# Performance work log

Hardware: AMD Instinct MI355X
Metric: run time of the kernel (lower is better)

The kernel has to match this reference:

```python
import jax, jax.numpy as jnp
import numpy as np


def setup_inputs() -> dict:
    key = jax.random.key(0)
    ks = jax.random.split(key, 7)
    B, T, I, H, O = 128, 1024, 256, 512, 128
    s_i = 1.0 / np.sqrt(I)
    s_h = 1.0 / np.sqrt(H)
    return {
        "x": jax.random.normal(ks[0], (B, T, I), dtype=jnp.float32),
        "W_ih": jax.random.normal(ks[1], (3 * H, I), dtype=jnp.float32) * s_i,
        "W_hh": jax.random.normal(ks[2], (3 * H, H), dtype=jnp.float32) * s_h,
        "b_ih": jax.random.normal(ks[3], (3 * H,), dtype=jnp.float32) * s_h,
        "b_hh": jax.random.normal(ks[4], (3 * H,), dtype=jnp.float32) * s_h,
        "fc_W": jax.random.normal(ks[5], (O, H), dtype=jnp.float32) * s_h,
        "fc_b": jax.random.normal(ks[6], (O,), dtype=jnp.float32) * s_h,
    }


def reference(x, W_ih, W_hh, b_ih, b_hh, fc_W, fc_b):
    # x: [B, T, I]. Standard torch GRUCell recurrence, scanned over time.
    B = x.shape[0]
    H = W_hh.shape[1]
    h0 = jnp.zeros((B, H), dtype=x.dtype)

    def step(h, xt):
        gx = xt @ W_ih.T + b_ih            # [B, 3H]
        gh = h @ W_hh.T + b_hh             # [B, 3H]
        gx_r, gx_z, gx_n = jnp.split(gx, 3, axis=-1)
        gh_r, gh_z, gh_n = jnp.split(gh, 3, axis=-1)
        r = jax.nn.sigmoid(gx_r + gh_r)
        z = jax.nn.sigmoid(gx_z + gh_z)
        n = jnp.tanh(gx_n + r * gh_n)
        h_new = (1.0 - z) * n + z * h
        return h_new, None

    xs = jnp.swapaxes(x, 0, 1)             # [T, B, I]
    h_last, _ = jax.lax.scan(step, h0, xs)
    return h_last @ fc_W.T + fc_b          # [B, O]
```

## Files before the change

### kernel.cpp

```cpp
#include <hip/hip_runtime.h>

#define B_ 128
#define T_ 1024
#define I_ 256
#define H_ 512
#define O_ 128

#define BGROUPS 4
#define ROWS 32
#define CGROUPS 32
#define HC 16
#define NBLK (BGROUPS*CGROUPS)
#define NTHR 512

#define HSLAB (B_*(H_/2))
#define FLAGS_OFF (2*HSLAB)
#define WS_INIT_BYTES ((2*HSLAB + T_*BGROUPS*CGROUPS)*4)

#define LDS_BYTES 32768

typedef __attribute__((ext_vector_type(8))) short short8;
typedef __attribute__((ext_vector_type(4))) float f32x4;

__device__ __forceinline__ unsigned int bf16rne(float f) {
    unsigned int u = __builtin_bit_cast(unsigned int, f);
    u += 0x7fffu + ((u >> 16) & 1u);
    return u >> 16;
}
__device__ __forceinline__ short8 pack8(float4 a, float4 b) {
    short8 r;
    r[0]=(short)bf16rne(a.x); r[1]=(short)bf16rne(a.y); r[2]=(short)bf16rne(a.z); r[3]=(short)bf16rne(a.w);
    r[4]=(short)bf16rne(b.x); r[5]=(short)bf16rne(b.y); r[6]=(short)bf16rne(b.z); r[7]=(short)bf16rne(b.w);
    return r;
}
__device__ __forceinline__ short8 cvt8(const float* p) {
    return pack8(*(const float4*)p, *(const float4*)(p + 4));
}

__global__ __launch_bounds__(NTHR, 1)
void gru_mfma(const float* __restrict__ x,
              const float* __restrict__ Wih,
              const float* __restrict__ Whh,
              const float* __restrict__ bih,
              const float* __restrict__ bhh,
              unsigned int* __restrict__ hslab,
              unsigned int* __restrict__ flags)
{
    __shared__ __align__(16) char smem[LDS_BYTES];

    const int tid  = threadIdx.x;
    const int lane = tid & 63;
    const int g    = blockIdx.x >> 5;
    const int cg   = blockIdx.x & 31;
    const int rb0  = g * ROWS;
    const int hc0  = cg * HC;

    const int wv = tid >> 6;
    const int mt = wv & 1;
    const int kq = wv >> 1;

    short8 BX[2][3], BH[4][3];
#pragma unroll
    for (int xk = 0; xk < 2; ++xk) {
        int kb = (kq * 2 + xk) * 32 + ((lane >> 4) << 3);
#pragma unroll
        for (int nt = 0; nt < 3; ++nt)
            BX[xk][nt] = cvt8(Wih + (nt * H_ + hc0 + (lane & 15)) * I_ + kb);
    }
#pragma unroll
    for (int hk = 0; hk < 4; ++hk) {
        int kb = (kq * 4 + hk) * 32 + ((lane >> 4) << 3);
#pragma unroll
        for (int nt = 0; nt < 3; ++nt)
            BH[hk][nt] = cvt8(Whh + (nt * H_ + hc0 + (lane & 15)) * H_ + kb);
    }

    const int arow = rb0 + mt * 16 + (lane & 15);
    const int kch  = lane >> 4;

    const int frow = tid >> 4;
    const int fcl  = tid & 15;
    const int j    = hc0 + fcl;
    const float bR  = bih[j] + bhh[j];
    const float bZ  = bih[H_ + j] + bhh[H_ + j];
    const float bNx = bih[2 * H_ + j];
    const float bNh = bhh[2 * H_ + j];
    const int mtf  = frow >> 4;
    const int r16  = frow & 15;
    const int fbase = ((((r16 >> 2) << 4) | fcl) << 2) + (r16 & 3);
    float hprev = 0.f;

    const float* xp0 = x + (arow * T_) * I_ + (kq * 2) * 32 + kch * 8;
    const float* xp1 = xp0 + 32;
    float4 pxa0 = *(const float4*)xp0, pxa1 = *(const float4*)(xp0 + 4);
    float4 pxb0 = *(const float4*)xp1, pxb1 = *(const float4*)(xp1 + 4);
    xp0 += I_; xp1 += I_;

#pragma unroll 1
    for (int t = 0; t < T_; ++t) {
        if (t > 0) {
            const unsigned int* fl = flags + ((t - 1) * BGROUPS + g) * CGROUPS;
            if (tid < 64) {
                unsigned int v;
                do {
                    v = __hip_atomic_load(fl + (lane & 31), __ATOMIC_RELAXED, __HIP_MEMORY_SCOPE_AGENT);
                } while (!__all((int)(v != 0)));
            }
        }
        __syncthreads();

        const unsigned int* hrowp = hslab + (t & 1) * HSLAB + arow * (H_ / 2) + kch * 4;
        unsigned long long hq[8];
#pragma unroll
        for (int hk = 0; hk < 4; ++hk) {
            const unsigned long long* p =
                (const unsigned long long*)(hrowp + (kq * 4 + hk) * 16);
            hq[2 * hk]     = __hip_atomic_load(p,     __ATOMIC_RELAXED, __HIP_MEMORY_SCOPE_AGENT);
            hq[2 * hk + 1] = __hip_atomic_load(p + 1, __ATOMIC_RELAXED, __HIP_MEMORY_SCOPE_AGENT);
        }

        f32x4 accR = {0.f, 0.f, 0.f, 0.f}, accZ = accR, accNX = accR, accNH = accR;
        {
            short8 ax0 = pack8(pxa0, pxa1);
            short8 ax1 = pack8(pxb0, pxb1);
            accR  = __builtin_amdgcn_mfma_f32_16x16x32_bf16(ax0, BX[0][0], accR, 0, 0, 0);
            accZ  = __builtin_amdgcn_mfma_f32_16x16x32_bf16(ax0, BX[0][1], accZ, 0, 0, 0);
            accNX = __builtin_amdgcn_mfma_f32_16x16x32_bf16(ax0, BX[0][2], accNX, 0, 0, 0);
            accR  = __builtin_amdgcn_mfma_f32_16x16x32_bf16(ax1, BX[1][0], accR, 0, 0, 0);
            accZ  = __builtin_amdgcn_mfma_f32_16x16x32_bf16(ax1, BX[1][1], accZ, 0, 0, 0);
            accNX = __builtin_amdgcn_mfma_f32_16x16x32_bf16(ax1, BX[1][2], accNX, 0, 0, 0);
        }
#pragma unroll
        for (int hk = 0; hk < 4; ++hk) {
            union { unsigned long long q[2]; short8 s; } u;
            u.q[0] = hq[2 * hk]; u.q[1] = hq[2 * hk + 1];
            accR  = __builtin_amdgcn_mfma_f32_16x16x32_bf16(u.s, BH[hk][0], accR, 0, 0, 0);
            accZ  = __builtin_amdgcn_mfma_f32_16x16x32_bf16(u.s, BH[hk][1], accZ, 0, 0, 0);
            accNH = __builtin_amdgcn_mfma_f32_16x16x32_bf16(u.s, BH[hk][2], accNH, 0, 0, 0);
        }

        {
            char* cb = smem + wv * 1024 + lane * 16;
            *(f32x4*)(cb +     0) = accR;
            *(f32x4*)(cb +  8192) = accZ;
            *(f32x4*)(cb + 16384) = accNX;
            *(f32x4*)(cb + 24576) = accNH;
        }
        __syncthreads();

        {
            const float* CB = (const float*)smem;
            float sr = bR, sz = bZ, sxn = bNx, shn = bNh;
#pragma unroll
            for (int q = 0; q < 4; ++q) {
                int base = (q * 2 + mtf) * 256 + fbase;
                sr  += CB[base];
                sz  += CB[2048 + base];
                sxn += CB[4096 + base];
                shn += CB[6144 + base];
            }
            float r = 1.f / (1.f + __expf(-sr));
            float z = 1.f / (1.f + __expf(-sz));
            float e2 = __expf(2.f * (sxn + r * shn));
            float n = 1.f - 2.f / (e2 + 1.f);
            float hnew = (1.f - z) * n + z * hprev;
            hprev = hnew;
            unsigned int hb = bf16rne(hnew);
            unsigned int ob = (unsigned int)__shfl_xor((int)hb, 1);
            if (!(fcl & 1)) {
                unsigned int pk = (hb & 0xffffu) | (ob << 16);
                __hip_atomic_store(hslab + ((t + 1) & 1) * HSLAB + (rb0 + frow) * (H_ / 2) + (j >> 1),
                                   pk, __ATOMIC_RELAXED, __HIP_MEMORY_SCOPE_AGENT);
            }
        }
        __syncthreads();

        if (tid == 0)
            __hip_atomic_store(flags + (t * BGROUPS + g) * CGROUPS + cg, 1u,
                               __ATOMIC_RELAXED, __HIP_MEMORY_SCOPE_AGENT);
        if (t + 1 < T_) {
            pxa0 = *(const float4*)xp0; pxa1 = *(const float4*)(xp0 + 4);
            pxb0 = *(const float4*)xp1; pxb1 = *(const float4*)(xp1 + 4);
            xp0 += I_; xp1 += I_;
        }
    }
}

__global__ __launch_bounds__(256)
void fc_kernel(const unsigned int* __restrict__ hp,
               const float* __restrict__ fcW,
               const float* __restrict__ fcb,
               float* __restrict__ out)
{
    int gid = blockIdx.x * 256 + threadIdx.x;
    int b = gid >> 7, o = gid & 127;
    const unsigned int* hr = hp + b * (H_ / 2);
    const float* wr = fcW + o * H_;
    float acc = 0.f;
#pragma unroll 8
    for (int i = 0; i < H_ / 2; i += 4) {
        uint4 v = *(const uint4*)(hr + i);
        float4 w0 = *(const float4*)(wr + 2 * i);
        float4 w1 = *(const float4*)(wr + 2 * i + 4);
        acc += __builtin_bit_cast(float, v.x << 16)          * w0.x
             + __builtin_bit_cast(float, v.x & 0xffff0000u)  * w0.y
             + __builtin_bit_cast(float, v.y << 16)          * w0.z
             + __builtin_bit_cast(float, v.y & 0xffff0000u)  * w0.w
             + __builtin_bit_cast(float, v.z << 16)          * w1.x
             + __builtin_bit_cast(float, v.z & 0xffff0000u)  * w1.y
             + __builtin_bit_cast(float, v.w << 16)          * w1.z
             + __builtin_bit_cast(float, v.w & 0xffff0000u)  * w1.w;
    }
    out[gid] = acc + fcb[o];
}

extern "C" void kernel_launch(void* const* d_in, const int* in_sizes, int n_in,
                              void* d_out, int out_size, void* d_ws, size_t ws_size,
                              hipStream_t stream)
{
    const float* x   = (const float*)d_in[0];
    const float* Wih = (const float*)d_in[1];
    const float* Whh = (const float*)d_in[2];
    const float* bih = (const float*)d_in[3];
    const float* bhh = (const float*)d_in[4];
    const float* fcW = (const float*)d_in[5];
    const float* fcb = (const float*)d_in[6];
    float* out = (float*)d_out;

    unsigned int* hslab = (unsigned int*)d_ws;
    unsigned int* flags = hslab + FLAGS_OFF;

    hipMemsetAsync(d_ws, 0, WS_INIT_BYTES, stream);

    hipLaunchKernelGGL(gru_mfma, dim3(NBLK), dim3(NTHR), 0, stream,
                       x, Wih, Whh, bih, bhh, hslab, flags);

    hipLaunchKernelGGL(fc_kernel, dim3((B_ * O_) / 256), dim3(256), 0, stream,
                       hslab, fcW, fcb, out);
}
```

Baseline: 4.016 ms.

## Replace per-step flag barrier with step-tagged 64-bit hidden-state words

Each packed bf16 pair of the hidden state is now stored in a 64-bit word whose upper half holds the timestep, so consumers spin directly on the data they need instead of polling a separate flag array and then reading the hidden state. This removes the producer-side barrier plus flag store and the consumer flag-poll round trip from each recurrent step, and each wave only waits on its own slice. In exchange, hidden-state traffic doubles and each lane issues more atomic loads. The FC kernel is adapted to skip the tag halves.

Result: slower. 7.746 ms (+92.9%).

```diff
diff --git a/kernel.cpp b/kernel.cpp
--- a/kernel.cpp
+++ b/kernel.cpp
@@ -13,9 +13,8 @@
 #define NBLK (BGROUPS*CGROUPS)
 #define NTHR 512
 
-#define HSLAB (B_*(H_/2))
-#define FLAGS_OFF (2*HSLAB)
-#define WS_INIT_BYTES ((2*HSLAB + T_*BGROUPS*CGROUPS)*4)
+#define HSLAB64 (B_*(H_/2))
+#define WS_INIT_BYTES (2*HSLAB64*8)
 
 #define LDS_BYTES 32768
 
@@ -35,6 +34,9 @@
 }
 __device__ __forceinline__ short8 cvt8(const float* p) {
     return pack8(*(const float4*)p, *(const float4*)(p + 4));
+}
+__device__ __forceinline__ unsigned long long ald64(const unsigned long long* p) {
+    return __hip_atomic_load(p, __ATOMIC_RELAXED, __HIP_MEMORY_SCOPE_AGENT);
 }
 
 __global__ __launch_bounds__(NTHR, 1)
@@ -43,8 +45,7 @@
               const float* __restrict__ Whh,
               const float* __restrict__ bih,
               const float* __restrict__ bhh,
-              unsigned int* __restrict__ hslab,
-              unsigned int* __restrict__ flags)
+              unsigned long long* __restrict__ hslab)
 {
     __shared__ __align__(16) char smem[LDS_BYTES];
 
@@ -96,27 +97,31 @@
     float4 pxb0 = *(const float4*)xp1, pxb1 = *(const float4*)(xp1 + 4);
     xp0 += I_; xp1 += I_;
 
+    const int hfo = arow * (H_ / 2) + kch * 4;
+
 #pragma unroll 1
     for (int t = 0; t < T_; ++t) {
-        if (t > 0) {
-            const unsigned int* fl = flags + ((t - 1) * BGROUPS + g) * CGROUPS;
-            if (tid < 64) {
-                unsigned int v;
-                do {
-                    v = __hip_atomic_load(fl + (lane & 31), __ATOMIC_RELAXED, __HIP_MEMORY_SCOPE_AGENT);
-                } while (!__all((int)(v != 0)));
-            }
-        }
-        __syncthreads();
-
-        const unsigned int* hrowp = hslab + (t & 1) * HSLAB + arow * (H_ / 2) + kch * 4;
-        unsigned long long hq[8];
+        const unsigned long long* hb64 = hslab + (t & 1) * HSLAB64 + hfo;
+        const unsigned int want = (unsigned int)t;
+        unsigned long long v[16];
 #pragma unroll
         for (int hk = 0; hk < 4; ++hk) {
-            const unsigned long long* p =
-                (const unsigned long long*)(hrowp + (kq * 4 + hk) * 16);
-            hq[2 * hk]     = __hip_atomic_load(p,     __ATOMIC_RELAXED, __HIP_MEMORY_SCOPE_AGENT);
-            hq[2 * hk + 1] = __hip_atomic_load(p + 1, __ATOMIC_RELAXED, __HIP_MEMORY_SCOPE_AGENT);
+            const unsigned long long* p = hb64 + (kq * 4 + hk) * 16;
+            v[4*hk+0] = ald64(p + 0);
+            v[4*hk+1] = ald64(p + 1);
+            v[4*hk+2] = ald64(p + 2);
+            v[4*hk+3] = ald64(p + 3);
+        }
+        for (;;) {
+            bool ok = true;
+#pragma unroll
+            for (int i = 0; i < 16; ++i)
+                if ((unsigned int)(v[i] >> 32) != want) ok = false;
+            if (ok) break;
+#pragma unroll
+            for (int i = 0; i < 16; ++i)
+                if ((unsigned int)(v[i] >> 32) != want)
+                    v[i] = ald64(hb64 + ((i >> 2) + kq * 4) * 16 + (i & 3));
         }
 
         f32x4 accR = {0.f, 0.f, 0.f, 0.f}, accZ = accR, accNX = accR, accNH = accR;
@@ -132,13 +137,17 @@
         }
 #pragma unroll
         for (int hk = 0; hk < 4; ++hk) {
-            union { unsigned long long q[2]; short8 s; } u;
-            u.q[0] = hq[2 * hk]; u.q[1] = hq[2 * hk + 1];
+            union { unsigned int w[4]; short8 s; } u;
+            u.w[0] = (unsigned int)v[4*hk+0];
+            u.w[1] = (unsigned int)v[4*hk+1];
+            u.w[2] = (unsigned int)v[4*hk+2];
+            u.w[3] = (unsigned int)v[4*hk+3];
             accR  = __builtin_amdgcn_mfma_f32_16x16x32_bf16(u.s, BH[hk][0], accR, 0, 0, 0);
             accZ  = __builtin_amdgcn_mfma_f32_16x16x32_bf16(u.s, BH[hk][1], accZ, 0, 0, 0);
             accNH = __builtin_amdgcn_mfma_f32_16x16x32_bf16(u.s, BH[hk][2], accNH, 0, 0, 0);
         }
 
+        __syncthreads();
         {
             char* cb = smem + wv * 1024 + lane * 16;
             *(f32x4*)(cb +     0) = accR;
@@ -168,16 +177,13 @@
             unsigned int hb = bf16rne(hnew);
             unsigned int ob = (unsigned int)__shfl_xor((int)hb, 1);
             if (!(fcl & 1)) {
-                unsigned int pk = (hb & 0xffffu) | (ob << 16);
-                __hip_atomic_store(hslab + ((t + 1) & 1) * HSLAB + (rb0 + frow) * (H_ / 2) + (j >> 1),
+                unsigned long long pk = (unsigned long long)((hb & 0xffffu) | ((ob & 0xffffu) << 16))
+                                      | ((unsigned long long)(unsigned int)(t + 1) << 32);
+                __hip_atomic_store(hslab + ((t + 1) & 1) * HSLAB64 + (rb0 + frow) * (H_ / 2) + (j >> 1),
                                    pk, __ATOMIC_RELAXED, __HIP_MEMORY_SCOPE_AGENT);
             }
         }
-        __syncthreads();
-
-        if (tid == 0)
-            __hip_atomic_store(flags + (t * BGROUPS + g) * CGROUPS + cg, 1u,
-                               __ATOMIC_RELAXED, __HIP_MEMORY_SCOPE_AGENT);
+
         if (t + 1 < T_) {
             pxa0 = *(const float4*)xp0; pxa1 = *(const float4*)(xp0 + 4);
             pxb0 = *(const float4*)xp1; pxb1 = *(const float4*)(xp1 + 4);
@@ -187,29 +193,24 @@
 }
 
 __global__ __launch_bounds__(256)
-void fc_kernel(const unsigned int* __restrict__ hp,
+void fc_kernel(const unsigned long long* __restrict__ hp,
                const float* __restrict__ fcW,
                const float* __restrict__ fcb,
                float* __restrict__ out)
 {
     int gid = blockIdx.x * 256 + threadIdx.x;
     int b = gid >> 7, o = gid & 127;
-    const unsigned int* hr = hp + b * (H_ / 2);
+    const unsigned long long* hr = hp + b * (H_ / 2);
     const float* wr = fcW + o * H_;
     float acc = 0.f;
 #pragma unroll 8
-    for (int i = 0; i < H_ / 2; i += 4) {
+    for (int i = 0; i < H_ / 2; i += 2) {
         uint4 v = *(const uint4*)(hr + i);
-        float4 w0 = *(const float4*)(wr + 2 * i);
-        float4 w1 = *(const float4*)(wr + 2 * i + 4);
-        acc += __builtin_bit_cast(float, v.x << 16)          * w0.x
-             + __builtin_bit_cast(float, v.x & 0xffff0000u)  * w0.y
-             + __builtin_bit_cast(float, v.y << 16)          * w0.z
-             + __builtin_bit_cast(float, v.y & 0xffff0000u)  * w0.w
-             + __builtin_bit_cast(float, v.z << 16)          * w1.x
-             + __builtin_bit_cast(float, v.z & 0xffff0000u)  * w1.y
-             + __builtin_bit_cast(float, v.w << 16)          * w1.z
-             + __builtin_bit_cast(float, v.w & 0xffff0000u)  * w1.w;
+        float4 w = *(const float4*)(wr + 2 * i);
+        acc += __builtin_bit_cast(float, v.x << 16)          * w.x
+             + __builtin_bit_cast(float, v.x & 0xffff0000u)  * w.y
+             + __builtin_bit_cast(float, v.z << 16)          * w.z
+             + __builtin_bit_cast(float, v.z & 0xffff0000u)  * w.w;
     }
     out[gid] = acc + fcb[o];
 }
@@ -227,13 +228,12 @@
     const float* fcb = (const float*)d_in[6];
     float* out = (float*)d_out;
 
-    unsigned int* hslab = (unsigned int*)d_ws;
-    unsigned int* flags = hslab + FLAGS_OFF;
+    unsigned long long* hslab = (unsigned long long*)d_ws;
 
     hipMemsetAsync(d_ws, 0, WS_INIT_BYTES, stream);
 
     hipLaunchKernelGGL(gru_mfma, dim3(NBLK), dim3(NTHR), 0, stream,
-                       x, Wih, Whh, bih, bhh, hslab, flags);
+                       x, Wih, Whh, bih, bhh, hslab);
 
     hipLaunchKernelGGL(fc_kernel, dim3((B_ * O_) / 256), dim3(256), 0, stream,
                        hslab, fcW, fcb, out);
```

## Halve block count, widen column tiles, use per-wave flags instead of block barriers

Applied to the files above, without the earlier changes.

Cuts the persistent grid from 128 to 64 blocks, each owning 32 hidden columns. Waves are split into two K-halves that reduce through a small LDS exchange, replacing the 8-way LDS reduction across all threads. Each epilogue wave now writes its own h tile and publishes a per-wave flag after a vmcnt wait, so two block-wide __syncthreads per step go away and every wave polls all 64 flags itself. The trade-off is more register pressure (twice the resident weight fragments), fewer CUs doing work, and heavier flag polling, since every wave reads all the flags.

New measurement: 7.215 ms. +79.6%, slower.

```diff
diff --git a/kernel.cpp b/kernel.cpp
--- a/kernel.cpp
+++ b/kernel.cpp
@@ -8,16 +8,14 @@
 
 #define BGROUPS 4
 #define ROWS 32
-#define CGROUPS 32
-#define HC 16
+#define CGROUPS 16
+#define HC 32
 #define NBLK (BGROUPS*CGROUPS)
 #define NTHR 512
 
-#define HSLAB (B_*(H_/2))
-#define FLAGS_OFF (2*HSLAB)
-#define WS_INIT_BYTES ((2*HSLAB + T_*BGROUPS*CGROUPS)*4)
-
-#define LDS_BYTES 32768
+#define HSLAB32 (B_*(H_/2))
+#define FLAGW 64
+#define WS_INIT_BYTES ((2*HSLAB32 + T_*BGROUPS*FLAGW)*4)
 
 typedef __attribute__((ext_vector_type(8))) short short8;
 typedef __attribute__((ext_vector_type(4))) float f32x4;
@@ -35,6 +33,9 @@
 }
 __device__ __forceinline__ short8 cvt8(const float* p) {
     return pack8(*(const float4*)p, *(const float4*)(p + 4));
+}
+__device__ __forceinline__ unsigned long long ald64(const unsigned long long* p) {
+    return __hip_atomic_load(p, __ATOMIC_RELAXED, __HIP_MEMORY_SCOPE_AGENT);
 }
 
 __global__ __launch_bounds__(NTHR, 1)
@@ -46,142 +47,146 @@
               unsigned int* __restrict__ hslab,
               unsigned int* __restrict__ flags)
 {
-    __shared__ __align__(16) char smem[LDS_BYTES];
+    __shared__ __align__(16) f32x4 cdump[4][4][64];
 
     const int tid  = threadIdx.x;
     const int lane = tid & 63;
-    const int g    = blockIdx.x >> 5;
-    const int cg   = blockIdx.x & 31;
+    const int g    = blockIdx.x >> 4;
+    const int cg   = blockIdx.x & 15;
     const int rb0  = g * ROWS;
     const int hc0  = cg * HC;
 
-    const int wv = tid >> 6;
-    const int mt = wv & 1;
-    const int kq = wv >> 1;
-
-    short8 BX[2][3], BH[4][3];
-#pragma unroll
-    for (int xk = 0; xk < 2; ++xk) {
-        int kb = (kq * 2 + xk) * 32 + ((lane >> 4) << 3);
+    const int wv   = tid >> 6;
+    const int mt   = wv & 1;
+    const int nh   = (wv >> 1) & 1;
+    const int kh   = wv >> 2;
+    const int pair = nh * 2 + mt;
+
+    const int coln = hc0 + nh * 16 + (lane & 15);
+    short8 BX[4][3], BH[8][3];
+#pragma unroll
+    for (int xk = 0; xk < 4; ++xk) {
+        int kb = kh * 128 + xk * 32 + ((lane >> 4) << 3);
 #pragma unroll
         for (int nt = 0; nt < 3; ++nt)
-            BX[xk][nt] = cvt8(Wih + (nt * H_ + hc0 + (lane & 15)) * I_ + kb);
-    }
-#pragma unroll
-    for (int hk = 0; hk < 4; ++hk) {
-        int kb = (kq * 4 + hk) * 32 + ((lane >> 4) << 3);
+            BX[xk][nt] = cvt8(Wih + (nt * H_ + coln) * I_ + kb);
+    }
+#pragma unroll
+    for (int hk = 0; hk < 8; ++hk) {
+        int kb = kh * 256 + hk * 32 + ((lane >> 4) << 3);
 #pragma unroll
         for (int nt = 0; nt < 3; ++nt)
-            BH[hk][nt] = cvt8(Whh + (nt * H_ + hc0 + (lane & 15)) * H_ + kb);
+            BH[hk][nt] = cvt8(Whh + (nt * H_ + coln) * H_ + kb);
     }
 
     const int arow = rb0 + mt * 16 + (lane & 15);
-    const int kch  = lane >> 4;
-
-    const int frow = tid >> 4;
-    const int fcl  = tid & 15;
-    const int j    = hc0 + fcl;
-    const float bR  = bih[j] + bhh[j];
-    const float bZ  = bih[H_ + j] + bhh[H_ + j];
-    const float bNx = bih[2 * H_ + j];
-    const float bNh = bhh[2 * H_ + j];
-    const int mtf  = frow >> 4;
-    const int r16  = frow & 15;
-    const int fbase = ((((r16 >> 2) << 4) | fcl) << 2) + (r16 & 3);
-    float hprev = 0.f;
-
-    const float* xp0 = x + (arow * T_) * I_ + (kq * 2) * 32 + kch * 8;
-    const float* xp1 = xp0 + 32;
-    float4 pxa0 = *(const float4*)xp0, pxa1 = *(const float4*)(xp0 + 4);
-    float4 pxb0 = *(const float4*)xp1, pxb1 = *(const float4*)(xp1 + 4);
-    xp0 += I_; xp1 += I_;
+    const int hfo  = arow * (H_ / 2) + ((lane >> 4) << 2);
+
+    const float bR  = bih[coln] + bhh[coln];
+    const float bZ  = bih[H_ + coln] + bhh[H_ + coln];
+    const float bNx = bih[2 * H_ + coln];
+    const float bNh = bhh[2 * H_ + coln];
+    float hprev[4] = {0.f, 0.f, 0.f, 0.f};
+
+    const float* xbase = x + (arow * T_) * I_ + kh * 128 + ((lane >> 4) << 3);
+    float4 px[8];
+#pragma unroll
+    for (int xk = 0; xk < 4; ++xk) {
+        px[2*xk]   = *(const float4*)(xbase + xk * 32);
+        px[2*xk+1] = *(const float4*)(xbase + xk * 32 + 4);
+    }
+    xbase += I_;
 
 #pragma unroll 1
     for (int t = 0; t < T_; ++t) {
         if (t > 0) {
-            const unsigned int* fl = flags + ((t - 1) * BGROUPS + g) * CGROUPS;
-            if (tid < 64) {
-                unsigned int v;
-                do {
-                    v = __hip_atomic_load(fl + (lane & 31), __ATOMIC_RELAXED, __HIP_MEMORY_SCOPE_AGENT);
-                } while (!__all((int)(v != 0)));
-            }
-        }
-        __syncthreads();
-
-        const unsigned int* hrowp = hslab + (t & 1) * HSLAB + arow * (H_ / 2) + kch * 4;
-        unsigned long long hq[8];
-#pragma unroll
-        for (int hk = 0; hk < 4; ++hk) {
-            const unsigned long long* p =
-                (const unsigned long long*)(hrowp + (kq * 4 + hk) * 16);
-            hq[2 * hk]     = __hip_atomic_load(p,     __ATOMIC_RELAXED, __HIP_MEMORY_SCOPE_AGENT);
-            hq[2 * hk + 1] = __hip_atomic_load(p + 1, __ATOMIC_RELAXED, __HIP_MEMORY_SCOPE_AGENT);
-        }
-
-        f32x4 accR = {0.f, 0.f, 0.f, 0.f}, accZ = accR, accNX = accR, accNH = accR;
-        {
-            short8 ax0 = pack8(pxa0, pxa1);
-            short8 ax1 = pack8(pxb0, pxb1);
-            accR  = __builtin_amdgcn_mfma_f32_16x16x32_bf16(ax0, BX[0][0], accR, 0, 0, 0);
-            accZ  = __builtin_amdgcn_mfma_f32_16x16x32_bf16(ax0, BX[0][1], accZ, 0, 0, 0);
-            accNX = __builtin_amdgcn_mfma_f32_16x16x32_bf16(ax0, BX[0][2], accNX, 0, 0, 0);
-            accR  = __builtin_amdgcn_mfma_f32_16x16x32_bf16(ax1, BX[1][0], accR, 0, 0, 0);
-            accZ  = __builtin_amdgcn_mfma_f32_16x16x32_bf16(ax1, BX[1][1], accZ, 0, 0, 0);
-            accNX = __builtin_amdgcn_mfma_f32_16x16x32_bf16(ax1, BX[1][2], accNX, 0, 0, 0);
-        }
-#pragma unroll
-        for (int hk = 0; hk < 4; ++hk) {
+            const unsigned int* fl = flags + ((t - 1) * BGROUPS + g) * FLAGW;
+            unsigned int fv;
+            do {
+                fv = __hip_atomic_load(fl + lane, __ATOMIC_RELAXED, __HIP_MEMORY_SCOPE_AGENT);
+            } while (!__all((int)(fv != 0)));
+        }
+        asm volatile("" ::: "memory");
+
+        const unsigned int* hb = hslab + (t & 1) * HSLAB32 + hfo;
+        unsigned long long hv[16];
+#pragma unroll
+        for (int hk = 0; hk < 8; ++hk) {
+            const unsigned long long* p = (const unsigned long long*)(hb + (kh * 8 + hk) * 16);
+            hv[2*hk]   = ald64(p);
+            hv[2*hk+1] = ald64(p + 1);
+        }
+
+        f32x4 accR = {0.f,0.f,0.f,0.f}, accZ = accR, accNX = accR, accNH = accR;
+#pragma unroll
+        for (int xk = 0; xk < 4; ++xk) {
+            short8 ax = pack8(px[2*xk], px[2*xk+1]);
+            accR  = __builtin_amdgcn_mfma_f32_16x16x32_bf16(ax, BX[xk][0], accR, 0, 0, 0);
+            accZ  = __builtin_amdgcn_mfma_f32_16x16x32_bf16(ax, BX[xk][1], accZ, 0, 0, 0);
+            accNX = __builtin_amdgcn_mfma_f32_16x16x32_bf16(ax, BX[xk][2], accNX, 0, 0, 0);
+        }
+#pragma unroll
+        for (int hk = 0; hk < 8; ++hk) {
             union { unsigned long long q[2]; short8 s; } u;
-            u.q[0] = hq[2 * hk]; u.q[1] = hq[2 * hk + 1];
+            u.q[0] = hv[2*hk]; u.q[1] = hv[2*hk+1];
             accR  = __builtin_amdgcn_mfma_f32_16x16x32_bf16(u.s, BH[hk][0], accR, 0, 0, 0);
             accZ  = __builtin_amdgcn_mfma_f32_16x16x32_bf16(u.s, BH[hk][1], accZ, 0, 0, 0);
             accNH = __builtin_amdgcn_mfma_f32_16x16x32_bf16(u.s, BH[hk][2], accNH, 0, 0, 0);
         }
 
-        {
-            char* cb = smem + wv * 1024 + lane * 16;
-            *(f32x4*)(cb +     0) = accR;
-            *(f32x4*)(cb +  8192) = accZ;
-            *(f32x4*)(cb + 16384) = accNX;
-            *(f32x4*)(cb + 24576) = accNH;
+        if (kh == 1) {
+            cdump[pair][0][lane] = accR;
+            cdump[pair][1][lane] = accZ;
+            cdump[pair][2][lane] = accNX;
+            cdump[pair][3][lane] = accNH;
         }
         __syncthreads();
 
-        {
-            const float* CB = (const float*)smem;
-            float sr = bR, sz = bZ, sxn = bNx, shn = bNh;
-#pragma unroll
-            for (int q = 0; q < 4; ++q) {
-                int base = (q * 2 + mtf) * 256 + fbase;
-                sr  += CB[base];
-                sz  += CB[2048 + base];
-                sxn += CB[4096 + base];
-                shn += CB[6144 + base];
+        if (kh == 0) {
+            f32x4 pR  = cdump[pair][0][lane];
+            f32x4 pZ  = cdump[pair][1][lane];
+            f32x4 pNX = cdump[pair][2][lane];
+            f32x4 pNH = cdump[pair][3][lane];
+            unsigned int hb16[4];
+#pragma unroll
+            for (int i = 0; i < 4; ++i) {
+                float sr  = accR[i]  + pR[i]  + bR;
+                float sz  = accZ[i]  + pZ[i]  + bZ;
+                float sxn = accNX[i] + pNX[i] + bNx;
+                float shn = accNH[i] + pNH[i] + bNh;
+                float r = 1.f / (1.f + __expf(-sr));
+                float z = 1.f / (1.f + __expf(-sz));
+                float e2 = __expf(2.f * (sxn + r * shn));
+                float n = 1.f - 2.f / (e2 + 1.f);
+                float hnew = (1.f - z) * n + z * hprev[i];
+                hprev[i] = hnew;
+                hb16[i] = bf16rne(hnew);
             }
-            float r = 1.f / (1.f + __expf(-sr));
-            float z = 1.f / (1.f + __expf(-sz));
-            float e2 = __expf(2.f * (sxn + r * shn));
-            float n = 1.f - 2.f / (e2 + 1.f);
-            float hnew = (1.f - z) * n + z * hprev;
-            hprev = hnew;
-            unsigned int hb = bf16rne(hnew);
-            unsigned int ob = (unsigned int)__shfl_xor((int)hb, 1);
-            if (!(fcl & 1)) {
-                unsigned int pk = (hb & 0xffffu) | (ob << 16);
-                __hip_atomic_store(hslab + ((t + 1) & 1) * HSLAB + (rb0 + frow) * (H_ / 2) + (j >> 1),
-                                   pk, __ATOMIC_RELAXED, __HIP_MEMORY_SCOPE_AGENT);
+            unsigned int* hdst = hslab + ((t + 1) & 1) * HSLAB32;
+            const int cw   = cg * 16 + nh * 8 + ((lane & 15) >> 1);
+            const int rowb = rb0 + mt * 16 + ((lane >> 4) << 2);
+#pragma unroll
+            for (int i = 0; i < 4; ++i) {
+                unsigned int ob = (unsigned int)__shfl_xor((int)hb16[i], 1);
+                if (!(lane & 1)) {
+                    __hip_atomic_store(hdst + (rowb + i) * (H_ / 2) + cw,
+                                       (hb16[i] & 0xffffu) | (ob << 16),
+                                       __ATOMIC_RELAXED, __HIP_MEMORY_SCOPE_AGENT);
+                }
             }
-        }
-        __syncthreads();
-
-        if (tid == 0)
-            __hip_atomic_store(flags + (t * BGROUPS + g) * CGROUPS + cg, 1u,
-                               __ATOMIC_RELAXED, __HIP_MEMORY_SCOPE_AGENT);
+            asm volatile("s_waitcnt vmcnt(0)" ::: "memory");
+            if (lane == 0)
+                __hip_atomic_store(flags + (t * BGROUPS + g) * FLAGW + cg * 4 + pair, 1u,
+                                   __ATOMIC_RELAXED, __HIP_MEMORY_SCOPE_AGENT);
+        }
+
         if (t + 1 < T_) {
-            pxa0 = *(const float4*)xp0; pxa1 = *(const float4*)(xp0 + 4);
-            pxb0 = *(const float4*)xp1; pxb1 = *(const float4*)(xp1 + 4);
-            xp0 += I_; xp1 += I_;
+#pragma unroll
+            for (int xk = 0; xk < 4; ++xk) {
+                px[2*xk]   = *(const float4*)(xbase + xk * 32);
+                px[2*xk+1] = *(const float4*)(xbase + xk * 32 + 4);
+            }
+            xbase += I_;
         }
     }
 }
@@ -228,7 +233,7 @@
     float* out = (float*)d_out;
 
     unsigned int* hslab = (unsigned int*)d_ws;
-    unsigned int* flags = hslab + FLAGS_OFF;
+    unsigned int* flags = hslab + 2 * HSLAB32;
 
     hipMemsetAsync(d_ws, 0, WS_INIT_BYTES, stream);
 
```

## Repartition GRU blocks into 8 batch groups by 16 hidden-column groups

Applied to the files above, without the earlier changes.

Changes the block decomposition from 4 batch groups of 32 rows × 32 column groups of 16 hidden units to 8 batch groups of 16 rows × 16 column groups of 32 hidden units. Each wave now covers 16 rows by 16 columns, using its half of the tile's columns instead of its half of the rows. The per-step flag barrier now waits on only 16 producer blocks instead of 32, which is meant to cut cross-block synchronisation latency on the serial time loop. The per-block Whh and Wih column slices double, and each block reads only 16 rows of h per step.

After: 4.264 ms. 6.2% more time.

```diff
diff --git a/kernel.cpp b/kernel.cpp
--- a/kernel.cpp
+++ b/kernel.cpp
@@ -6,18 +6,15 @@
 #define H_ 512
 #define O_ 128
 
-#define BGROUPS 4
-#define ROWS 32
-#define CGROUPS 32
-#define HC 16
+#define BGROUPS 8
+#define ROWS 16
+#define CGROUPS 16
+#define HC 32
 #define NBLK (BGROUPS*CGROUPS)
 #define NTHR 512
 
-#define HSLAB (B_*(H_/2))
-#define FLAGS_OFF (2*HSLAB)
-#define WS_INIT_BYTES ((2*HSLAB + T_*BGROUPS*CGROUPS)*4)
-
-#define LDS_BYTES 32768
+#define HSLAB32 (B_*(H_/2))
+#define WS_INIT_BYTES ((2*HSLAB32 + T_*BGROUPS*CGROUPS)*4)
 
 typedef __attribute__((ext_vector_type(8))) short short8;
 typedef __attribute__((ext_vector_type(4))) float f32x4;
@@ -35,6 +32,9 @@
 }
 __device__ __forceinline__ short8 cvt8(const float* p) {
     return pack8(*(const float4*)p, *(const float4*)(p + 4));
+}
+__device__ __forceinline__ unsigned long long ald64(const unsigned long long* p) {
+    return __hip_atomic_load(p, __ATOMIC_RELAXED, __HIP_MEMORY_SCOPE_AGENT);
 }
 
 __global__ __launch_bounds__(NTHR, 1)
@@ -46,118 +46,111 @@
               unsigned int* __restrict__ hslab,
               unsigned int* __restrict__ flags)
 {
-    __shared__ __align__(16) char smem[LDS_BYTES];
+    __shared__ __align__(16) float CB[8][4][256];
 
     const int tid  = threadIdx.x;
     const int lane = tid & 63;
-    const int g    = blockIdx.x >> 5;
-    const int cg   = blockIdx.x & 31;
+    const int g    = blockIdx.x >> 4;
+    const int cg   = blockIdx.x & 15;
     const int rb0  = g * ROWS;
     const int hc0  = cg * HC;
 
     const int wv = tid >> 6;
-    const int mt = wv & 1;
+    const int nh = wv & 1;
     const int kq = wv >> 1;
 
+    const int coln = hc0 + nh * 16 + (lane & 15);
     short8 BX[2][3], BH[4][3];
 #pragma unroll
     for (int xk = 0; xk < 2; ++xk) {
-        int kb = (kq * 2 + xk) * 32 + ((lane >> 4) << 3);
+        int kb = kq * 64 + xk * 32 + ((lane >> 4) << 3);
 #pragma unroll
         for (int nt = 0; nt < 3; ++nt)
-            BX[xk][nt] = cvt8(Wih + (nt * H_ + hc0 + (lane & 15)) * I_ + kb);
+            BX[xk][nt] = cvt8(Wih + (nt * H_ + coln) * I_ + kb);
     }
 #pragma unroll
     for (int hk = 0; hk < 4; ++hk) {
-        int kb = (kq * 4 + hk) * 32 + ((lane >> 4) << 3);
+        int kb = kq * 128 + hk * 32 + ((lane >> 4) << 3);
 #pragma unroll
         for (int nt = 0; nt < 3; ++nt)
-            BH[hk][nt] = cvt8(Whh + (nt * H_ + hc0 + (lane & 15)) * H_ + kb);
-    }
-
-    const int arow = rb0 + mt * 16 + (lane & 15);
-    const int kch  = lane >> 4;
-
-    const int frow = tid >> 4;
-    const int fcl  = tid & 15;
+            BH[hk][nt] = cvt8(Whh + (nt * H_ + coln) * H_ + kb);
+    }
+
+    const int arow = rb0 + (lane & 15);
+    const int hfo  = arow * (H_ / 2) + ((lane >> 4) << 2);
+
+    const int frow = tid >> 5;
+    const int fcl  = tid & 31;
     const int j    = hc0 + fcl;
     const float bR  = bih[j] + bhh[j];
     const float bZ  = bih[H_ + j] + bhh[H_ + j];
     const float bNx = bih[2 * H_ + j];
     const float bNh = bhh[2 * H_ + j];
-    const int mtf  = frow >> 4;
-    const int r16  = frow & 15;
-    const int fbase = ((((r16 >> 2) << 4) | fcl) << 2) + (r16 & 3);
+    const int nh_f  = fcl >> 4;
+    const int fbase = ((((frow >> 2) << 4) | (fcl & 15)) << 2) + (frow & 3);
     float hprev = 0.f;
 
-    const float* xp0 = x + (arow * T_) * I_ + (kq * 2) * 32 + kch * 8;
-    const float* xp1 = xp0 + 32;
-    float4 pxa0 = *(const float4*)xp0, pxa1 = *(const float4*)(xp0 + 4);
-    float4 pxb0 = *(const float4*)xp1, pxb1 = *(const float4*)(xp1 + 4);
-    xp0 += I_; xp1 += I_;
+    const float* xptr = x + (arow * T_) * I_ + kq * 64 + ((lane >> 4) << 3);
+    float4 px[4];
+    px[0] = *(const float4*)xptr;        px[1] = *(const float4*)(xptr + 4);
+    px[2] = *(const float4*)(xptr + 32); px[3] = *(const float4*)(xptr + 36);
+    xptr += I_;
 
 #pragma unroll 1
     for (int t = 0; t < T_; ++t) {
-        if (t > 0) {
+        if (t > 0 && tid < 64) {
             const unsigned int* fl = flags + ((t - 1) * BGROUPS + g) * CGROUPS;
-            if (tid < 64) {
-                unsigned int v;
-                do {
-                    v = __hip_atomic_load(fl + (lane & 31), __ATOMIC_RELAXED, __HIP_MEMORY_SCOPE_AGENT);
-                } while (!__all((int)(v != 0)));
-            }
+            unsigned int fv;
+            do {
+                fv = __hip_atomic_load(fl + (lane & 15), __ATOMIC_RELAXED, __HIP_MEMORY_SCOPE_AGENT);
+            } while (!__all((int)(fv != 0)));
         }
         __syncthreads();
 
-        const unsigned int* hrowp = hslab + (t & 1) * HSLAB + arow * (H_ / 2) + kch * 4;
-        unsigned long long hq[8];
+        const unsigned int* hb = hslab + (t & 1) * HSLAB32 + hfo;
+        unsigned long long hv[8];
 #pragma unroll
         for (int hk = 0; hk < 4; ++hk) {
-            const unsigned long long* p =
-                (const unsigned long long*)(hrowp + (kq * 4 + hk) * 16);
-            hq[2 * hk]     = __hip_atomic_load(p,     __ATOMIC_RELAXED, __HIP_MEMORY_SCOPE_AGENT);
-            hq[2 * hk + 1] = __hip_atomic_load(p + 1, __ATOMIC_RELAXED, __HIP_MEMORY_SCOPE_AGENT);
-        }
-
-        f32x4 accR = {0.f, 0.f, 0.f, 0.f}, accZ = accR, accNX = accR, accNH = accR;
-        {
-            short8 ax0 = pack8(pxa0, pxa1);
-            short8 ax1 = pack8(pxb0, pxb1);
-            accR  = __builtin_amdgcn_mfma_f32_16x16x32_bf16(ax0, BX[0][0], accR, 0, 0, 0);
-            accZ  = __builtin_amdgcn_mfma_f32_16x16x32_bf16(ax0, BX[0][1], accZ, 0, 0, 0);
-            accNX = __builtin_amdgcn_mfma_f32_16x16x32_bf16(ax0, BX[0][2], accNX, 0, 0, 0);
-            accR  = __builtin_amdgcn_mfma_f32_16x16x32_bf16(ax1, BX[1][0], accR, 0, 0, 0);
-            accZ  = __builtin_amdgcn_mfma_f32_16x16x32_bf16(ax1, BX[1][1], accZ, 0, 0, 0);
-            accNX = __builtin_amdgcn_mfma_f32_16x16x32_bf16(ax1, BX[1][2], accNX, 0, 0, 0);
+            const unsigned long long* p = (const unsigned long long*)(hb + (kq * 4 + hk) * 16);
+            hv[2*hk]   = ald64(p);
+            hv[2*hk+1] = ald64(p + 1);
+        }
+
+        f32x4 accR = {0.f,0.f,0.f,0.f}, accZ = accR, accNX = accR, accNH = accR;
+#pragma unroll
+        for (int xk = 0; xk < 2; ++xk) {
+            short8 ax = pack8(px[2*xk], px[2*xk+1]);
+            accR  = __builtin_amdgcn_mfma_f32_16x16x32_bf16(ax, BX[xk][0], accR, 0, 0, 0);
+            accZ  = __builtin_amdgcn_mfma_f32_16x16x32_bf16(ax, BX[xk][1], accZ, 0, 0, 0);
+            accNX = __builtin_amdgcn_mfma_f32_16x16x32_bf16(ax, BX[xk][2], accNX, 0, 0, 0);
         }
 #pragma unroll
         for (int hk = 0; hk < 4; ++hk) {
             union { unsigned long long q[2]; short8 s; } u;
-            u.q[0] = hq[2 * hk]; u.q[1] = hq[2 * hk + 1];
+            u.q[0] = hv[2*hk]; u.q[1] = hv[2*hk+1];
             accR  = __builtin_amdgcn_mfma_f32_16x16x32_bf16(u.s, BH[hk][0], accR, 0, 0, 0);
             accZ  = __builtin_amdgcn_mfma_f32_16x16x32_bf16(u.s, BH[hk][1], accZ, 0, 0, 0);
             accNH = __builtin_amdgcn_mfma_f32_16x16x32_bf16(u.s, BH[hk][2], accNH, 0, 0, 0);
         }
 
         {
-            char* cb = smem + wv * 1024 + lane * 16;
-            *(f32x4*)(cb +     0) = accR;
-            *(f32x4*)(cb +  8192) = accZ;
-            *(f32x4*)(cb + 16384) = accNX;
-            *(f32x4*)(cb + 24576) = accNH;
+            float* cb = &CB[wv][0][0] + lane * 4;
+            *(f32x4*)(cb +   0) = accR;
+            *(f32x4*)(cb + 256) = accZ;
+            *(f32x4*)(cb + 512) = accNX;
+            *(f32x4*)(cb + 768) = accNH;
         }
         __syncthreads();
 
         {
-            const float* CB = (const float*)smem;
             float sr = bR, sz = bZ, sxn = bNx, shn = bNh;
 #pragma unroll
             for (int q = 0; q < 4; ++q) {
-                int base = (q * 2 + mtf) * 256 + fbase;
-                sr  += CB[base];
-                sz  += CB[2048 + base];
-                sxn += CB[4096 + base];
-                shn += CB[6144 + base];
+                const float* cb = &CB[q * 2 + nh_f][0][0] + fbase;
+                sr  += cb[0];
+                sz  += cb[256];
+                sxn += cb[512];
+                shn += cb[768];
             }
             float r = 1.f / (1.f + __expf(-sr));
             float z = 1.f / (1.f + __expf(-sz));
@@ -165,23 +158,24 @@
             float n = 1.f - 2.f / (e2 + 1.f);
             float hnew = (1.f - z) * n + z * hprev;
             hprev = hnew;
-            unsigned int hb = bf16rne(hnew);
-            unsigned int ob = (unsigned int)__shfl_xor((int)hb, 1);
+            unsigned int hb16 = bf16rne(hnew);
+            unsigned int ob = (unsigned int)__shfl_xor((int)hb16, 1);
             if (!(fcl & 1)) {
-                unsigned int pk = (hb & 0xffffu) | (ob << 16);
-                __hip_atomic_store(hslab + ((t + 1) & 1) * HSLAB + (rb0 + frow) * (H_ / 2) + (j >> 1),
-                                   pk, __ATOMIC_RELAXED, __HIP_MEMORY_SCOPE_AGENT);
+                __hip_atomic_store(hslab + ((t + 1) & 1) * HSLAB32 + (rb0 + frow) * (H_ / 2) + (j >> 1),
+                                   (hb16 & 0xffffu) | (ob << 16),
+                                   __ATOMIC_RELAXED, __HIP_MEMORY_SCOPE_AGENT);
             }
         }
+
         __syncthreads();
-
         if (tid == 0)
             __hip_atomic_store(flags + (t * BGROUPS + g) * CGROUPS + cg, 1u,
                                __ATOMIC_RELAXED, __HIP_MEMORY_SCOPE_AGENT);
+
         if (t + 1 < T_) {
-            pxa0 = *(const float4*)xp0; pxa1 = *(const float4*)(xp0 + 4);
-            pxb0 = *(const float4*)xp1; pxb1 = *(const float4*)(xp1 + 4);
-            xp0 += I_; xp1 += I_;
+            px[0] = *(const float4*)xptr;        px[1] = *(const float4*)(xptr + 4);
+            px[2] = *(const float4*)(xptr + 32); px[3] = *(const float4*)(xptr + 36);
+            xptr += I_;
         }
     }
 }
@@ -228,7 +222,7 @@
     float* out = (float*)d_out;
 
     unsigned int* hslab = (unsigned int*)d_ws;
-    unsigned int* flags = hslab + FLAGS_OFF;
+    unsigned int* flags = hslab + 2 * HSLAB32;
 
     hipMemsetAsync(d_ws, 0, WS_INIT_BYTES, stream);
 
```
